# Kernel optimization log

Measured on AMD Instinct MI355X. Metric: run time of the kernel, lower is better.

## Reference

```python
import jax, jax.numpy as jnp
import numpy as np
import math

N, IN_DIM, Z, H, OUT, K = 16384, 64, 128, 1, 3, 16


def setup_inputs() -> dict:
    key = jax.random.key(0)
    ks = jax.random.split(key, 16)

    def lin(k, din, dout):
        kw, kb = jax.random.split(k)
        W = jax.random.normal(kw, (din, dout), jnp.float32) / math.sqrt(din)
        b = jax.random.normal(kb, (dout,), jnp.float32) * 0.01
        return W, b

    x = jax.random.normal(ks[0], (N, IN_DIM), jnp.float32)
    t = jnp.zeros((1,), jnp.float32)
    # layer dims: (in, heads*out) per TransformerConv
    dims = [(IN_DIM, Z * H), (Z * H, (Z // H) * H), (Z * H, (OUT // H) * H)]
    params = {}
    i = 1
    for li, (din, dout) in enumerate(dims, 1):
        for nm in ("q", "k", "v", "s"):
            W, b = lin(ks[i], din, dout)
            i += 1
            params[f"W{nm}{li}"] = W
            params[f"b{nm}{li}"] = b
    return {"t": t, "x": x, **params}


def knn_edge_index(coo, k):
    # kNN graph on 3-D coords (loop=False): edges neighbor(src) -> center(dst)
    n = coo.shape[0]
    sq = jnp.sum(coo * coo, axis=-1)
    d = sq[:, None] + sq[None, :] - 2.0 * (coo @ coo.T)  # [N, N] sq. distances
    d = d.at[jnp.arange(n), jnp.arange(n)].set(jnp.inf)  # exclude self-loops
    _, idx = jax.lax.top_k(-d, k)  # [N, K] nearest neighbor indices
    src = idx.reshape(-1)
    dst = jnp.repeat(jnp.arange(n), k)
    return src, dst


def tconv(x, src, dst, Wq, bq, Wk, bk, Wv, bv, Ws, bs, heads):
    # PyG TransformerConv (concat=True, root_weight=True, no edge_attr)
    n = x.shape[0]
    dout = Wq.shape[1]
    c = dout // heads
    q = (x @ Wq + bq).reshape(n, heads, c)
    kk = (x @ Wk + bk).reshape(n, heads, c)
    v = (x @ Wv + bv).reshape(n, heads, c)
    alpha = jnp.sum(q[dst] * kk[src], axis=-1) / math.sqrt(c)  # [E, H]
    amax = jax.ops.segment_max(alpha, dst, num_segments=n)
    ex = jnp.exp(alpha - amax[dst])
    denom = jax.ops.segment_sum(ex, dst, num_segments=n)
    w = ex / denom[dst]  # softmax over incoming edges per node
    msg = w[:, :, None] * v[src]  # [E, H, C]
    out = jax.ops.segment_sum(msg, dst, num_segments=n).reshape(n, dout)
    return out + x @ Ws + bs  # root/skip connection


def reference(t, x,
              Wq1, bq1, Wk1, bk1, Wv1, bv1, Ws1, bs1,
              Wq2, bq2, Wk2, bk2, Wv2, bv2, Ws2, bs2,
              Wq3, bq3, Wk3, bk3, Wv3, bv3, Ws3, bs3):
    src, dst = knn_edge_index(x[:, :3], K)  # built under no_grad in original
    h = jnp.tanh(tconv(x, src, dst, Wq1, bq1, Wk1, bk1, Wv1, bv1, Ws1, bs1, H))
    h = jnp.tanh(tconv(h, src, dst, Wq2, bq2, Wk2, bk2, Wv2, bv2, Ws2, bs2, H) + h)
    drift_coo = tconv(h, src, dst, Wq3, bq3, Wk3, bk3, Wv3, bv3, Ws3, bs3, H)
    return drift_coo
```

## Files before the change

### kernel.cpp

```cpp
#include <hip/hip_runtime.h>
#include <math.h>

#define NN 16384
#define QPW 2
#define CAP 128
#define WM 64
#define KTOP 17

typedef unsigned long long u64;

__global__ __launch_bounds__(256) void pack_coords(const float* __restrict__ x,
                                                   float4* __restrict__ coo) {
  int i = blockIdx.x * 256 + threadIdx.x;
  float a = x[i * 64 + 0];
  float b = x[i * 64 + 1];
  float c = x[i * 64 + 2];
  coo[i] = make_float4(a, b, c, a * a + b * b + c * c);
}

__device__ __forceinline__ int mbcnt64(u64 mask) {
  return __builtin_amdgcn_mbcnt_hi(
      (unsigned)(mask >> 32),
      __builtin_amdgcn_mbcnt_lo((unsigned)mask, 0));
}

__device__ __forceinline__ unsigned fmap(float d) {
  unsigned ub = __float_as_uint(d);
  return ub ^ ((unsigned)((int)ub >> 31) | 0x80000000u);
}

__device__ __forceinline__ float unfmap(unsigned ub) {
  unsigned fb = (ub & 0x80000000u) ? (ub ^ 0x80000000u) : ~ub;
  return __uint_as_float(fb);
}

__device__ __forceinline__ unsigned short f2bf(float f) {
  unsigned u = __float_as_uint(f);
  return (unsigned short)((u + 0x7FFFu + ((u >> 16) & 1u)) >> 16);
}

__device__ __forceinline__ float fast_tanh(float x) {
  const float e = __expf(-2.0f * fabsf(x));
  const float t = (1.0f - e) / (1.0f + e);
  return copysignf(t, x);
}

__device__ __forceinline__ u64 u64min(u64 a, u64 b) { return a < b ? a : b; }
__device__ __forceinline__ u64 u64max(u64 a, u64 b) { return a > b ? a : b; }

__device__ __forceinline__ void sort128(u64& r0, u64& r1, int lane) {
#pragma unroll
  for (int k = 2; k <= 128; k <<= 1) {
    if (k == 128) {
      u64 lo = u64min(r0, r1);
      r1 = u64max(r0, r1);
      r0 = lo;
    }
#pragma unroll
    for (int jj = (k == 128 ? 32 : (k >> 1)); jj >= 1; jj >>= 1) {
      const bool up = (lane & jj) == 0;
      const bool asc0 = (lane & k) == 0;
      const bool asc1 = ((lane | 64) & k) == 0;
      u64 o0 = __shfl_xor(r0, jj);
      u64 o1 = __shfl_xor(r1, jj);
      r0 = (up == asc0) ? u64min(r0, o0) : u64max(r0, o0);
      r1 = (up == asc1) ? u64min(r1, o1) : u64max(r1, o1);
    }
  }
}

__device__ __forceinline__ void radix_shrink(u64* buf, int& cnt, float& th,
                                             int lane) {
  const u64 k0 = (lane < cnt) ? buf[lane] : ~0ull;
  const u64 k1 = (lane + 64 < cnt) ? buf[lane + 64] : ~0ull;
  const unsigned d0 = (unsigned)(k0 >> 32);
  const unsigned d1 = (unsigned)(k1 >> 32);
  unsigned p = 0u;
#pragma unroll
  for (int b = 31; b >= 0; --b) {
    const unsigned c = p | (1u << b);
    const u64 b0 = __ballot(d0 < c);
    const u64 b1 = __ballot(d1 < c);
    const int n = __popcll(b0) + __popcll(b1);
    if (n < KTOP) p = c;
  }
  const bool v0 = d0 <= p;
  const bool v1 = d1 <= p;
  const u64 m0 = __ballot(v0);
  const u64 m1 = __ballot(v1);
  const int base = __popcll(m0);
  if (v0) buf[mbcnt64(m0)] = k0;
  if (v1) buf[base + mbcnt64(m1)] = k1;
  cnt = base + __popcll(m1);
  th = unfmap(p);
}

__global__ __launch_bounds__(256) void knn_kernel(const float4* __restrict__ coo,
                                                  int* __restrict__ src) {
  __shared__ u64 bufs[4][QPW][CAP];
  const int lane = threadIdx.x & 63;
  const int wid = threadIdx.x >> 6;
  const int node0 = blockIdx.x * (4 * QPW) + wid * QPW;

  float nx[QPW], ny[QPW], nz[QPW], sq[QPW], th[QPW];
  int cnt[QPW];
#pragma unroll
  for (int q = 0; q < QPW; ++q) {
    const float4 me = coo[node0 + q];
    nx[q] = -2.0f * me.x;
    ny[q] = -2.0f * me.y;
    nz[q] = -2.0f * me.z;
    sq[q] = me.w;
    cnt[q] = 0;
  }

  {
    const float4 pa = coo[lane];
    const float4 pb = coo[64 + lane];
#pragma unroll
    for (int q = 0; q < QPW; ++q) {
      const float d0 = sq[q] + fmaf(nx[q], pa.x,
                           fmaf(ny[q], pa.y, fmaf(nz[q], pa.z, pa.w)));
      const float d1 = sq[q] + fmaf(nx[q], pb.x,
                           fmaf(ny[q], pb.y, fmaf(nz[q], pb.z, pb.w)));
      bufs[wid][q][lane] = ((u64)fmap(d0) << 32) | (unsigned)lane;
      bufs[wid][q][64 + lane] = ((u64)fmap(d1) << 32) | (unsigned)(64 + lane);
      cnt[q] = 128;
      radix_shrink(bufs[wid][q], cnt[q], th[q], lane);
    }
  }

  float4 s0 = coo[2 * 64 + lane];
  float4 s1 = coo[3 * 64 + lane];
  float4 s2 = coo[4 * 64 + lane];
  float4 s3 = coo[5 * 64 + lane];

  auto body = [&](const float4 cur, const int step) {
    const int j = step * 64 + lane;
    float dd[QPW];
#pragma unroll
    for (int q = 0; q < QPW; ++q)
      dd[q] = sq[q] + fmaf(nx[q], cur.x,
                           fmaf(ny[q], cur.y, fmaf(nz[q], cur.z, cur.w)));
    u64 mk[QPW];
#pragma unroll
    for (int q = 0; q < QPW; ++q) mk[q] = __ballot(dd[q] <= th[q]);
    if (mk[0] | mk[1]) {
#pragma unroll
      for (int q = 0; q < QPW; ++q) {
        if (mk[q]) {
          if (dd[q] <= th[q])
            bufs[wid][q][cnt[q] + mbcnt64(mk[q])] =
                ((u64)fmap(dd[q]) << 32) | (unsigned)j;
          cnt[q] += __popcll(mk[q]);
          if (cnt[q] >= WM) radix_shrink(bufs[wid][q], cnt[q], th[q], lane);
        }
      }
    }
  };

#pragma unroll 1
  for (int g = 0; g < 63; ++g) {
    const int base = 2 + g * 4;
    body(s0, base + 0);
    s0 = coo[(base + 4) * 64 + lane];
    body(s1, base + 1);
    s1 = coo[(base + 5) * 64 + lane];
    body(s2, base + 2);
    s2 = coo[(base + 6) * 64 + lane];
    body(s3, base + 3);
    s3 = coo[(base + 7) * 64 + lane];
  }
  body(s0, 254);
  body(s1, 255);

#pragma unroll 1
  for (int q = 0; q < QPW; ++q) {
    u64 r0 = (lane < cnt[q]) ? bufs[wid][q][lane] : ~0ull;
    u64 r1 = (lane + 64 < cnt[q]) ? bufs[wid][q][lane + 64] : ~0ull;
    sort128(r0, r1, lane);
    const int idx = (int)(r0 & 0xFFFFFFFFull);
    const u64 selfm = __ballot((lane < KTOP) && (idx == node0 + q));
    const int s = selfm ? (__ffsll((long long)selfm) - 1) : 99;
    const int outrank = lane - (lane > s ? 1 : 0);
    if (lane < KTOP && lane != s && outrank < 16)
      src[(node0 + q) * 16 + outrank] = idx;
  }
}

template <int KD>
__global__ __launch_bounds__(256) void gemm_qkvs(
    const float* __restrict__ X, const float* __restrict__ W0,
    const float* __restrict__ W1, const float* __restrict__ W2,
    const float* __restrict__ W3, const float* __restrict__ B0,
    const float* __restrict__ B1, const float* __restrict__ B2,
    const float* __restrict__ B3, float* __restrict__ qs,
    unsigned short* __restrict__ kvh) {
  __shared__ float As[64][68];
  __shared__ float Bs[64][64];
  const int brow = blockIdx.x * 64;
  const int by = blockIdx.y;
  const int wi = by >> 1;
  const float* W = wi == 0 ? W0 : wi == 1 ? W1 : wi == 2 ? W2 : W3;
  const float* bias = wi == 0 ? B0 : wi == 1 ? B1 : wi == 2 ? B2 : B3;
  const int cbase = (by & 1) * 64;
  const int tx = threadIdx.x & 15;
  const int ty = threadIdx.x >> 4;

  float acc[4][4] = {};
  for (int k0 = 0; k0 < KD; k0 += 64) {
    __syncthreads();
#pragma unroll
    for (int i = 0; i < 4; ++i) {
      const int flat = threadIdx.x * 4 + i * 1024;
      const int r = flat >> 6, kk = flat & 63;
      const float4 v = *(const float4*)&X[(brow + r) * KD + k0 + kk];
      As[kk + 0][r] = v.x;
      As[kk + 1][r] = v.y;
      As[kk + 2][r] = v.z;
      As[kk + 3][r] = v.w;
    }
#pragma unroll
    for (int i = 0; i < 4; ++i) {
      const int flat = threadIdx.x * 4 + i * 1024;
      const int kk = flat >> 6, c = flat & 63;
      *(float4*)&Bs[kk][c] = *(const float4*)&W[(k0 + kk) * 128 + cbase + c];
    }
    __syncthreads();
#pragma unroll 8
    for (int k = 0; k < 64; ++k) {
      const float4 a = *(const float4*)&As[k][ty * 4];
      const float4 b = *(const float4*)&Bs[k][tx * 4];
      const float av[4] = {a.x, a.y, a.z, a.w};
      const float bv[4] = {b.x, b.y, b.z, b.w};
#pragma unroll
      for (int i = 0; i < 4; ++i)
#pragma unroll
        for (int jj = 0; jj < 4; ++jj)
          acc[i][jj] = fmaf(av[i], bv[jj], acc[i][jj]);
    }
  }
  const float4 bi = *(const float4*)&bias[cbase + tx * 4];
  const int col = cbase + tx * 4;
#pragma unroll
  for (int i = 0; i < 4; ++i) {
    const int row = brow + ty * 4 + i;
    float4 o;
    o.x = acc[i][0] + bi.x;
    o.y = acc[i][1] + bi.y;
    o.z = acc[i][2] + bi.z;
    o.w = acc[i][3] + bi.w;
    if (wi == 0) {
      *(float4*)&qs[row * 256 + col] = o;
    } else if (wi == 3) {
      *(float4*)&qs[row * 256 + 128 + col] = o;
    } else {
      ushort4 h;
      h.x = f2bf(o.x);
      h.y = f2bf(o.y);
      h.z = f2bf(o.z);
      h.w = f2bf(o.w);
      *(ushort4*)&kvh[row * 256 + col * 2 + (wi == 1 ? 0 : 4)] = h;
    }
  }
}

__global__ __launch_bounds__(256) void attn_c128(
    const float* __restrict__ qs, const unsigned short* __restrict__ kvh,
    const int* __restrict__ src, const float* __restrict__ res,
    float* __restrict__ hout, int do_res) {
  const int g = threadIdx.x >> 5;
  const int node = blockIdx.x * 8 + g;
  const int c = threadIdx.x & 31;
  const float4 q4 = ((const float4*)(qs + node * 256))[c];

  int nb[16];
#pragma unroll
  for (int r = 0; r < 16; ++r) nb[r] = src[node * 16 + r];

  float p[16];
  unsigned vlo[16], vhi[16];
#pragma unroll
  for (int r = 0; r < 16; ++r) {
    const uint4 kv = ((const uint4*)(kvh + nb[r] * 256))[c];
    const float k0 = __uint_as_float(kv.x << 16);
    const float k1 = __uint_as_float(kv.x & 0xFFFF0000u);
    const float k2 = __uint_as_float(kv.y << 16);
    const float k3 = __uint_as_float(kv.y & 0xFFFF0000u);
    p[r] = q4.x * k0 + q4.y * k1 + q4.z * k2 + q4.w * k3;
    vlo[r] = kv.z;
    vhi[r] = kv.w;
  }
#pragma unroll
  for (int o = 16; o; o >>= 1) {
#pragma unroll
    for (int r = 0; r < 16; ++r) p[r] += __shfl_xor(p[r], o);
  }

  float m = p[0];
#pragma unroll
  for (int r = 1; r < 16; ++r) m = fmaxf(m, p[r]);
  float w[16];
  float den = 0.0f;
#pragma unroll
  for (int r = 0; r < 16; ++r) {
    w[r] = __expf((p[r] - m) * 0.088388347648318447f);
    den += w[r];
  }
  const float inv = 1.0f / den;
  float o0 = 0.0f, o1 = 0.0f, o2 = 0.0f, o3 = 0.0f;
#pragma unroll
  for (int r = 0; r < 16; ++r) {
    const float ww = w[r] * inv;
    o0 = fmaf(ww, __uint_as_float(vlo[r] << 16), o0);
    o1 = fmaf(ww, __uint_as_float(vlo[r] & 0xFFFF0000u), o1);
    o2 = fmaf(ww, __uint_as_float(vhi[r] << 16), o2);
    o3 = fmaf(ww, __uint_as_float(vhi[r] & 0xFFFF0000u), o3);
  }
  const float4 s4 = ((const float4*)(qs + node * 256 + 128))[c];
  float r0 = o0 + s4.x, r1 = o1 + s4.y, r2 = o2 + s4.z, r3 = o3 + s4.w;
  if (do_res) {
    const float4 h4 = ((const float4*)(res + node * 128))[c];
    r0 += h4.x;
    r1 += h4.y;
    r2 += h4.z;
    r3 += h4.w;
  }
  ((float4*)(hout + node * 128))[c] = make_float4(
      fast_tanh(r0), fast_tanh(r1), fast_tanh(r2), fast_tanh(r3));
}

__global__ __launch_bounds__(256) void gemm_qkvs3(
    const float* __restrict__ H, const float* __restrict__ W0,
    const float* __restrict__ W1, const float* __restrict__ W2,
    const float* __restrict__ W3, const float* __restrict__ B0,
    const float* __restrict__ B1, const float* __restrict__ B2,
    const float* __restrict__ B3, float* __restrict__ out) {
  __shared__ float hs[64][132];
  __shared__ float wsh[128 * 12];
  __shared__ float bsh[12];
  const int brow = blockIdx.x * 64;
  if (threadIdx.x < 12) {
    const int mi = threadIdx.x / 3, c = threadIdx.x % 3;
    const float* Bsel = mi == 0 ? B0 : mi == 1 ? B1 : mi == 2 ? B2 : B3;
    bsh[threadIdx.x] = Bsel[c];
  }
  for (int t = threadIdx.x; t < 1536; t += 256) {
    const int k = t / 12, cc = t % 12;
    const int mi = cc / 3, c = cc % 3;
    const float* Wsel = mi == 0 ? W0 : mi == 1 ? W1 : mi == 2 ? W2 : W3;
    wsh[t] = Wsel[k * 3 + c];
  }
#pragma unroll
  for (int i = 0; i < 8; ++i) {
    const int flat = threadIdx.x * 4 + i * 1024;
    const int r = flat >> 7, kk = flat & 127;
    *(float4*)&hs[r][kk] = *(const float4*)&H[(brow + r) * 128 + kk];
  }
  __syncthreads();
  const int r = threadIdx.x >> 2;
  const int part = threadIdx.x & 3;
  float a0 = 0.0f, a1 = 0.0f, a2 = 0.0f;
#pragma unroll 4
  for (int k = 0; k < 128; ++k) {
    const float h = hs[r][k];
    a0 = fmaf(h, wsh[k * 12 + part * 3 + 0], a0);
    a1 = fmaf(h, wsh[k * 12 + part * 3 + 1], a1);
    a2 = fmaf(h, wsh[k * 12 + part * 3 + 2], a2);
  }
  const int row = brow + r;
  out[row * 12 + part * 3 + 0] = a0 + bsh[part * 3 + 0];
  out[row * 12 + part * 3 + 1] = a1 + bsh[part * 3 + 1];
  out[row * 12 + part * 3 + 2] = a2 + bsh[part * 3 + 2];
}

__global__ __launch_bounds__(256) void attn_c3(const float* __restrict__ q3,
                                               const int* __restrict__ src,
                                               float* __restrict__ out) {
  const int gid = blockIdx.x * 256 + threadIdx.x;
  const int node = gid >> 4, r = gid & 15;
  const int j = src[node * 16 + r];
  const float* qn = q3 + node * 12;
  const float* kj = q3 + j * 12 + 3;
  float alpha = (qn[0] * kj[0] + qn[1] * kj[1] + qn[2] * kj[2]) *
                0.57735026918962576f;
  float m = alpha;
#pragma unroll
  for (int o = 8; o; o >>= 1) m = fmaxf(m, __shfl_xor(m, o, 16));
  const float e = __expf(alpha - m);
  float den = e;
#pragma unroll
  for (int o = 8; o; o >>= 1) den += __shfl_xor(den, o, 16);
  const float wgt = e / den;
  const float* vj = q3 + j * 12 + 6;
  float o0 = wgt * vj[0], o1 = wgt * vj[1], o2 = wgt * vj[2];
#pragma unroll
  for (int o = 8; o; o >>= 1) {
    o0 += __shfl_xor(o0, o, 16);
    o1 += __shfl_xor(o1, o, 16);
    o2 += __shfl_xor(o2, o, 16);
  }
  if (r == 0) {
    const float* sn = q3 + node * 12 + 9;
    out[node * 3 + 0] = o0 + sn[0];
    out[node * 3 + 1] = o1 + sn[1];
    out[node * 3 + 2] = o2 + sn[2];
  }
}

extern "C" void kernel_launch(void* const* d_in, const int* in_sizes, int n_in,
                              void* d_out, int out_size, void* d_ws,
                              size_t ws_size, hipStream_t stream) {
  const float* x = (const float*)d_in[1];
  const float* Wq1 = (const float*)d_in[2];
  const float* bq1 = (const float*)d_in[3];
  const float* Wk1 = (const float*)d_in[4];
  const float* bk1 = (const float*)d_in[5];
  const float* Wv1 = (const float*)d_in[6];
  const float* bv1 = (const float*)d_in[7];
  const float* Ws1 = (const float*)d_in[8];
  const float* bs1 = (const float*)d_in[9];
  const float* Wq2 = (const float*)d_in[10];
  const float* bq2 = (const float*)d_in[11];
  const float* Wk2 = (const float*)d_in[12];
  const float* bk2 = (const float*)d_in[13];
  const float* Wv2 = (const float*)d_in[14];
  const float* bv2 = (const float*)d_in[15];
  const float* Ws2 = (const float*)d_in[16];
  const float* bs2 = (const float*)d_in[17];
  const float* Wq3 = (const float*)d_in[18];
  const float* bq3 = (const float*)d_in[19];
  const float* Wk3 = (const float*)d_in[20];
  const float* bk3 = (const float*)d_in[21];
  const float* Wv3 = (const float*)d_in[22];
  const float* bv3 = (const float*)d_in[23];
  const float* Ws3 = (const float*)d_in[24];
  const float* bs3 = (const float*)d_in[25];

  const size_t MB = 1024 * 1024;
  char* ws = (char*)d_ws;
  float* qs = (float*)(ws);
  unsigned short* kvh = (unsigned short*)(ws + 16 * MB);
  float* h1 = (float*)(ws + 24 * MB);
  float* h2 = (float*)(ws + 32 * MB);
  int* src = (int*)(ws + 40 * MB);
  float4* coo = (float4*)(ws + 41 * MB);
  float* q3 = (float*)(ws + 42 * MB);
  float* out = (float*)d_out;

  pack_coords<<<NN / 256, 256, 0, stream>>>(x, coo);
  knn_kernel<<<NN / (4 * QPW), 256, 0, stream>>>(coo, src);
  gemm_qkvs<64><<<dim3(NN / 64, 8), 256, 0, stream>>>(
      x, Wq1, Wk1, Wv1, Ws1, bq1, bk1, bv1, bs1, qs, kvh);
  attn_c128<<<NN / 8, 256, 0, stream>>>(qs, kvh, src, nullptr, h1, 0);
  gemm_qkvs<128><<<dim3(NN / 64, 8), 256, 0, stream>>>(
      h1, Wq2, Wk2, Wv2, Ws2, bq2, bk2, bv2, bs2, qs, kvh);
  attn_c128<<<NN / 8, 256, 0, stream>>>(qs, kvh, src, h1, h2, 1);
  gemm_qkvs3<<<NN / 64, 256, 0, stream>>>(h2, Wq3, Wk3, Wv3, Ws3, bq3, bk3,
                                          bv3, bs3, q3);
  attn_c3<<<NN * 16 / 256, 256, 0, stream>>>(q3, src, out);
}
```

Measured before the change: 307.0 us.

## Replace FP32 QKVS GEMMs with bf16 MFMA and store hidden states in bf16

Swaps the scalar FP32 shared-memory GEMMs for layers 1 and 2 with a bf16 MFMA 16x16x32 kernel. Each wave computes one 16x16 output tile, loading operands straight from global memory. New prep kernels convert x to bf16 and transpose and convert the weights, and the hidden activations h1/h2 are now stored in bf16 to feed the MFMA path and halve their traffic. This cuts GEMM compute time at the cost of extra prep launches, scattered scalar output stores, and lower precision in the projections and residuals.

```diff
diff --git a/kernel.cpp b/kernel.cpp
--- a/kernel.cpp
+++ b/kernel.cpp
@@ -8,6 +8,8 @@
 #define KTOP 17
 
 typedef unsigned long long u64;
+typedef __attribute__((ext_vector_type(8))) short bf16x8;
+typedef __attribute__((ext_vector_type(4))) float f32x4;
 
 __global__ __launch_bounds__(256) void pack_coords(const float* __restrict__ x,
                                                    float4* __restrict__ coo) {
@@ -37,6 +39,9 @@
 __device__ __forceinline__ unsigned short f2bf(float f) {
   unsigned u = __float_as_uint(f);
   return (unsigned short)((u + 0x7FFFu + ((u >> 16) & 1u)) >> 16);
+}
+__device__ __forceinline__ float bf2f(unsigned short h) {
+  return __uint_as_float(((unsigned)h) << 16);
 }
 
 __device__ __forceinline__ float fast_tanh(float x) {
@@ -188,87 +193,76 @@
   }
 }
 
+__global__ __launch_bounds__(256) void prep_xh(const float* __restrict__ x,
+                                               unsigned short* __restrict__ xh) {
+  const int i = (blockIdx.x * 256 + threadIdx.x) * 4;
+  const float4 v = *(const float4*)&x[i];
+  ushort4 h;
+  h.x = f2bf(v.x);
+  h.y = f2bf(v.y);
+  h.z = f2bf(v.z);
+  h.w = f2bf(v.w);
+  *(ushort4*)&xh[i] = h;
+}
+
+__global__ __launch_bounds__(256) void prep_wt(
+    const float* __restrict__ W0, const float* __restrict__ W1,
+    const float* __restrict__ W2, const float* __restrict__ W3,
+    const float* __restrict__ B0, const float* __restrict__ B1,
+    const float* __restrict__ B2, const float* __restrict__ B3, int KD,
+    unsigned short* __restrict__ WT, float* __restrict__ bias512) {
+  const int n = blockIdx.x;
+  const int wi = n >> 7, c = n & 127;
+  const float* W = wi == 0 ? W0 : wi == 1 ? W1 : wi == 2 ? W2 : W3;
+  const float* B = wi == 0 ? B0 : wi == 1 ? B1 : wi == 2 ? B2 : B3;
+  for (int k = threadIdx.x; k < KD; k += 256) WT[n * KD + k] = f2bf(W[k * 128 + c]);
+  if (threadIdx.x == 0) bias512[n] = B[c];
+}
+
 template <int KD>
-__global__ __launch_bounds__(256) void gemm_qkvs(
-    const float* __restrict__ X, const float* __restrict__ W0,
-    const float* __restrict__ W1, const float* __restrict__ W2,
-    const float* __restrict__ W3, const float* __restrict__ B0,
-    const float* __restrict__ B1, const float* __restrict__ B2,
-    const float* __restrict__ B3, float* __restrict__ qs,
+__global__ __launch_bounds__(256) void gemm_mfma(
+    const unsigned short* __restrict__ Xh, const unsigned short* __restrict__ WT,
+    const float* __restrict__ bias512, float* __restrict__ qs,
     unsigned short* __restrict__ kvh) {
-  __shared__ float As[64][68];
-  __shared__ float Bs[64][64];
-  const int brow = blockIdx.x * 64;
-  const int by = blockIdx.y;
-  const int wi = by >> 1;
-  const float* W = wi == 0 ? W0 : wi == 1 ? W1 : wi == 2 ? W2 : W3;
-  const float* bias = wi == 0 ? B0 : wi == 1 ? B1 : wi == 2 ? B2 : B3;
-  const int cbase = (by & 1) * 64;
-  const int tx = threadIdx.x & 15;
-  const int ty = threadIdx.x >> 4;
-
-  float acc[4][4] = {};
-  for (int k0 = 0; k0 < KD; k0 += 64) {
-    __syncthreads();
-#pragma unroll
-    for (int i = 0; i < 4; ++i) {
-      const int flat = threadIdx.x * 4 + i * 1024;
-      const int r = flat >> 6, kk = flat & 63;
-      const float4 v = *(const float4*)&X[(brow + r) * KD + k0 + kk];
-      As[kk + 0][r] = v.x;
-      As[kk + 1][r] = v.y;
-      As[kk + 2][r] = v.z;
-      As[kk + 3][r] = v.w;
-    }
-#pragma unroll
-    for (int i = 0; i < 4; ++i) {
-      const int flat = threadIdx.x * 4 + i * 1024;
-      const int kk = flat >> 6, c = flat & 63;
-      *(float4*)&Bs[kk][c] = *(const float4*)&W[(k0 + kk) * 128 + cbase + c];
-    }
-    __syncthreads();
-#pragma unroll 8
-    for (int k = 0; k < 64; ++k) {
-      const float4 a = *(const float4*)&As[k][ty * 4];
-      const float4 b = *(const float4*)&Bs[k][tx * 4];
-      const float av[4] = {a.x, a.y, a.z, a.w};
-      const float bv[4] = {b.x, b.y, b.z, b.w};
-#pragma unroll
-      for (int i = 0; i < 4; ++i)
-#pragma unroll
-        for (int jj = 0; jj < 4; ++jj)
-          acc[i][jj] = fmaf(av[i], bv[jj], acc[i][jj]);
-    }
-  }
-  const float4 bi = *(const float4*)&bias[cbase + tx * 4];
-  const int col = cbase + tx * 4;
-#pragma unroll
-  for (int i = 0; i < 4; ++i) {
-    const int row = brow + ty * 4 + i;
-    float4 o;
-    o.x = acc[i][0] + bi.x;
-    o.y = acc[i][1] + bi.y;
-    o.z = acc[i][2] + bi.z;
-    o.w = acc[i][3] + bi.w;
-    if (wi == 0) {
-      *(float4*)&qs[row * 256 + col] = o;
-    } else if (wi == 3) {
-      *(float4*)&qs[row * 256 + 128 + col] = o;
-    } else {
-      ushort4 h;
-      h.x = f2bf(o.x);
-      h.y = f2bf(o.y);
-      h.z = f2bf(o.z);
-      h.w = f2bf(o.w);
-      *(ushort4*)&kvh[row * 256 + col * 2 + (wi == 1 ? 0 : 4)] = h;
-    }
+  const int lane = threadIdx.x & 63;
+  const int wid = threadIdx.x >> 6;
+  const int m0 = (blockIdx.x * 4 + wid) * 16;
+  const int n0 = blockIdx.y * 16;
+  const int lm = lane & 15;
+  const int kq = (lane >> 4) * 8;
+
+  const unsigned short* arow = Xh + (size_t)(m0 + lm) * KD + kq;
+  const unsigned short* brow = WT + (size_t)(n0 + lm) * KD + kq;
+
+  f32x4 acc = {0.f, 0.f, 0.f, 0.f};
+#pragma unroll
+  for (int kk = 0; kk < KD / 32; ++kk) {
+    const bf16x8 a = *(const bf16x8*)(arow + kk * 32);
+    const bf16x8 b = *(const bf16x8*)(brow + kk * 32);
+    acc = __builtin_amdgcn_mfma_f32_16x16x32_bf16(a, b, acc, 0, 0, 0);
+  }
+
+  const int col = n0 + lm;
+  const float bv = bias512[col];
+  const int r0 = m0 + (lane >> 4) * 4;
+  const int wi = col >> 7;
+  const int c = col & 127;
+  if (wi == 0 || wi == 3) {
+    float* dst = qs + (wi == 0 ? c : 128 + c);
+#pragma unroll
+    for (int i = 0; i < 4; ++i) dst[(size_t)(r0 + i) * 256] = acc[i] + bv;
+  } else {
+    const int off = 8 * (c >> 2) + (c & 3) + (wi == 1 ? 0 : 4);
+#pragma unroll
+    for (int i = 0; i < 4; ++i)
+      kvh[(size_t)(r0 + i) * 256 + off] = f2bf(acc[i] + bv);
   }
 }
 
 __global__ __launch_bounds__(256) void attn_c128(
     const float* __restrict__ qs, const unsigned short* __restrict__ kvh,
-    const int* __restrict__ src, const float* __restrict__ res,
-    float* __restrict__ hout, int do_res) {
+    const int* __restrict__ src, const unsigned short* __restrict__ res,
+    unsigned short* __restrict__ hout, int do_res) {
   const int g = threadIdx.x >> 5;
   const int node = blockIdx.x * 8 + g;
   const int c = threadIdx.x & 31;
@@ -320,18 +314,22 @@
   const float4 s4 = ((const float4*)(qs + node * 256 + 128))[c];
   float r0 = o0 + s4.x, r1 = o1 + s4.y, r2 = o2 + s4.z, r3 = o3 + s4.w;
   if (do_res) {
-    const float4 h4 = ((const float4*)(res + node * 128))[c];
-    r0 += h4.x;
-    r1 += h4.y;
-    r2 += h4.z;
-    r3 += h4.w;
-  }
-  ((float4*)(hout + node * 128))[c] = make_float4(
-      fast_tanh(r0), fast_tanh(r1), fast_tanh(r2), fast_tanh(r3));
+    const ushort4 h4 = *(const ushort4*)&res[node * 128 + c * 4];
+    r0 += bf2f(h4.x);
+    r1 += bf2f(h4.y);
+    r2 += bf2f(h4.z);
+    r3 += bf2f(h4.w);
+  }
+  ushort4 ho;
+  ho.x = f2bf(fast_tanh(r0));
+  ho.y = f2bf(fast_tanh(r1));
+  ho.z = f2bf(fast_tanh(r2));
+  ho.w = f2bf(fast_tanh(r3));
+  *(ushort4*)&hout[node * 128 + c * 4] = ho;
 }
 
 __global__ __launch_bounds__(256) void gemm_qkvs3(
-    const float* __restrict__ H, const float* __restrict__ W0,
+    const unsigned short* __restrict__ H, const float* __restrict__ W0,
     const float* __restrict__ W1, const float* __restrict__ W2,
     const float* __restrict__ W3, const float* __restrict__ B0,
     const float* __restrict__ B1, const float* __restrict__ B2,
@@ -355,7 +353,11 @@
   for (int i = 0; i < 8; ++i) {
     const int flat = threadIdx.x * 4 + i * 1024;
     const int r = flat >> 7, kk = flat & 127;
-    *(float4*)&hs[r][kk] = *(const float4*)&H[(brow + r) * 128 + kk];
+    const ushort4 hv = *(const ushort4*)&H[(brow + r) * 128 + kk];
+    hs[r][kk + 0] = bf2f(hv.x);
+    hs[r][kk + 1] = bf2f(hv.y);
+    hs[r][kk + 2] = bf2f(hv.z);
+    hs[r][kk + 3] = bf2f(hv.w);
   }
   __syncthreads();
   const int r = threadIdx.x >> 2;
@@ -441,20 +443,28 @@
   char* ws = (char*)d_ws;
   float* qs = (float*)(ws);
   unsigned short* kvh = (unsigned short*)(ws + 16 * MB);
-  float* h1 = (float*)(ws + 24 * MB);
-  float* h2 = (float*)(ws + 32 * MB);
-  int* src = (int*)(ws + 40 * MB);
-  float4* coo = (float4*)(ws + 41 * MB);
-  float* q3 = (float*)(ws + 42 * MB);
+  unsigned short* h1 = (unsigned short*)(ws + 24 * MB);
+  unsigned short* h2 = (unsigned short*)(ws + 28 * MB);
+  int* src = (int*)(ws + 32 * MB);
+  float4* coo = (float4*)(ws + 33 * MB);
+  float* q3 = (float*)(ws + 34 * MB);
+  unsigned short* xh = (unsigned short*)(ws + 35 * MB);
+  unsigned short* wt1 = (unsigned short*)(ws + 37 * MB);
+  unsigned short* wt2 = (unsigned short*)(ws + 37 * MB + 256 * 1024);
+  float* b512_1 = (float*)(ws + 38 * MB);
+  float* b512_2 = (float*)(ws + 38 * MB + 16 * 1024);
   float* out = (float*)d_out;
 
   pack_coords<<<NN / 256, 256, 0, stream>>>(x, coo);
+  prep_xh<<<NN * 64 / 1024, 256, 0, stream>>>(x, xh);
+  prep_wt<<<512, 256, 0, stream>>>(Wq1, Wk1, Wv1, Ws1, bq1, bk1, bv1, bs1, 64,
+                                   wt1, b512_1);
+  prep_wt<<<512, 256, 0, stream>>>(Wq2, Wk2, Wv2, Ws2, bq2, bk2, bv2, bs2, 128,
+                                   wt2, b512_2);
   knn_kernel<<<NN / (4 * QPW), 256, 0, stream>>>(coo, src);
-  gemm_qkvs<64><<<dim3(NN / 64, 8), 256, 0, stream>>>(
-      x, Wq1, Wk1, Wv1, Ws1, bq1, bk1, bv1, bs1, qs, kvh);
+  gemm_mfma<64><<<dim3(NN / 64, 32), 256, 0, stream>>>(xh, wt1, b512_1, qs, kvh);
   attn_c128<<<NN / 8, 256, 0, stream>>>(qs, kvh, src, nullptr, h1, 0);
-  gemm_qkvs<128><<<dim3(NN / 64, 8), 256, 0, stream>>>(
-      h1, Wq2, Wk2, Wv2, Ws2, bq2, bk2, bv2, bs2, qs, kvh);
+  gemm_mfma<128><<<dim3(NN / 64, 32), 256, 0, stream>>>(h1, wt2, b512_2, qs, kvh);
   attn_c128<<<NN / 8, 256, 0, stream>>>(qs, kvh, src, h1, h2, 1);
   gemm_qkvs3<<<NN / 64, 256, 0, stream>>>(h2, Wq3, Wk3, Wv3, Ws3, bq3, bk3,
                                           bv3, bs3, q3);
```

After: 316.7 us. +3.2%, slower.
